# Performance work log

Measured on AMD Instinct MI355X. Metric: run time of the kernel, lower is better.

The kernel has to match this reference:

```python
import jax, jax.numpy as jnp
import numpy as np

def setup_inputs() -> dict:
    key = jax.random.key(0)
    k1, k2, k3, k4 = jax.random.split(key, 4)
    B, T, C, D = 4, 4096, 1024, 128
    x = jax.random.normal(k1, (B, T, C), dtype=jnp.float32)
    Wq = jax.random.normal(k2, (C, D), dtype=jnp.float32) * (C ** -0.5)
    Wk = jax.random.normal(k3, (C, D), dtype=jnp.float32) * (C ** -0.5)
    Wv = jax.random.normal(k4, (C, D), dtype=jnp.float32) * (C ** -0.5)
    return {"x": x, "Wq": Wq, "Wk": Wk, "Wv": Wv}

def reference(x, Wq, Wk, Wv):
    # x: [B,T,C]; Wq/Wk/Wv: [C,D] (nn.Linear bias=False => x @ W)
    B, T, C = x.shape
    q = jnp.einsum('btc,cd->btd', x, Wq)  # [B,T,D]
    k = jnp.einsum('btc,cd->btd', x, Wk)
    v = jnp.einsum('btc,cd->btd', x, Wv)
    dk = q.shape[-1]
    scale = dk ** -0.5
    w = jnp.einsum('btd,bsd->bts', q, k) * scale  # [B,T,T]
    causal = jnp.tril(jnp.ones((T, T), dtype=bool))
    w = jnp.where(causal, w, -jnp.inf)
    w = jax.nn.softmax(w, axis=-1)
    # dropout p=0.0 => identity
    attention = jnp.einsum('bts,bsd->btd', w, v)  # [B,T,D]
    return attention
```

## Files before the change

kernel.cpp:

```cpp
#include <hip/hip_runtime.h>
#include <stdint.h>

typedef __bf16 bf16_t;
typedef bf16_t bf16x8 __attribute__((ext_vector_type(8)));
typedef float f32x4 __attribute__((ext_vector_type(4)));
typedef unsigned short us8 __attribute__((ext_vector_type(8)));
typedef unsigned short us4 __attribute__((ext_vector_type(4)));

#define B_ 4
#define T_ 4096
#define C_ 1024
#define D_ 128

#define NCHUNK_PB 288
#define L2E 1.4426950408889634f

__device__ __forceinline__ uint16_t f2bf(float f) {
    union { float f; uint32_t u; } v; v.f = f;
    uint32_t u = v.u;
    uint32_t r = (u + 0x7fffu + ((u >> 16) & 1u)) >> 16;
    return (uint16_t)r;
}

__global__ __launch_bounds__(256) void prep_w(const float* __restrict__ Wq,
                                              const float* __restrict__ Wk,
                                              const float* __restrict__ Wv,
                                              uint16_t* __restrict__ WT) {
    int idx = blockIdx.x * 256 + threadIdx.x;
    if (idx >= 3 * D_ * C_) return;
    int w   = idx / (D_ * C_);
    int rem = idx - w * (D_ * C_);
    int n   = rem / C_;
    int k   = rem - n * C_;
    const float* W = (w == 0) ? Wq : (w == 1) ? Wk : Wv;
    WT[idx] = f2bf(W[(size_t)k * D_ + n]);
}

#define AST 40

__global__ __launch_bounds__(256) void qkv_gemm(const float* __restrict__ x,
                                                const uint16_t* __restrict__ WT,
                                                uint16_t* __restrict__ qb,
                                                uint16_t* __restrict__ kb,
                                                uint16_t* __restrict__ vT) {
    __shared__ __align__(16) uint16_t A_lds[32 * AST];
    __shared__ __align__(16) uint16_t W_lds[3][128 * AST];

    int tid  = threadIdx.x;
    int lane = tid & 63;
    int wave = tid >> 6;
    int quad = lane >> 4;
    int lx   = lane & 15;
    int wm   = wave >> 1, wn = wave & 1;
    int m0   = blockIdx.x * 32;

    f32x4 acc[3][4];
    for (int w = 0; w < 3; w++)
        for (int nf = 0; nf < 4; nf++)
            acc[w][nf] = (f32x4){0.f, 0.f, 0.f, 0.f};

    int arow = tid >> 3, acb = (tid & 7) * 4;

    for (int k0 = 0; k0 < C_; k0 += 32) {
        {
            float4 a = *(const float4*)(x + (size_t)(m0 + arow) * C_ + k0 + acb);
            us4 u;
            u[0] = f2bf(a.x); u[1] = f2bf(a.y); u[2] = f2bf(a.z); u[3] = f2bf(a.w);
            *(us4*)&A_lds[arow * AST + acb] = u;
        }
#pragma unroll
        for (int i = 0; i < 6; i++) {
            int f = i * 2048 + tid * 8;
            int w = f >> 12, n = (f >> 5) & 127, kk = f & 31;
            *(us8*)&W_lds[w][n * AST + kk] =
                *(const us8*)(WT + (size_t)w * (D_ * C_) + (size_t)n * C_ + k0 + kk);
        }
        __syncthreads();

        bf16x8 af = *(const bf16x8*)&A_lds[(wm * 16 + lx) * AST + quad * 8];
#pragma unroll
        for (int w = 0; w < 3; w++)
#pragma unroll
            for (int nf = 0; nf < 4; nf++) {
                bf16x8 bf = *(const bf16x8*)&W_lds[w][(wn * 64 + nf * 16 + lx) * AST + quad * 8];
                acc[w][nf] = __builtin_amdgcn_mfma_f32_16x16x32_bf16(af, bf, acc[w][nf], 0, 0, 0);
            }
        __syncthreads();
    }

    int mbase = m0 + wm * 16 + quad * 4;
#pragma unroll
    for (int nf = 0; nf < 4; nf++) {
        int n = wn * 64 + nf * 16 + lx;
#pragma unroll
        for (int r = 0; r < 4; r++)
            qb[(size_t)(mbase + r) * D_ + n] = f2bf(acc[0][nf][r]);
#pragma unroll
        for (int r = 0; r < 4; r++)
            kb[(size_t)(mbase + r) * D_ + n] = f2bf(acc[1][nf][r]);
        int batch = mbase >> 12;
        int t     = mbase & 4095;
        us4 pv;
        pv[0] = f2bf(acc[2][nf][0]);
        pv[1] = f2bf(acc[2][nf][1]);
        pv[2] = f2bf(acc[2][nf][2]);
        pv[3] = f2bf(acc[2][nf][3]);
        *(us4*)&vT[(size_t)batch * D_ * T_ + (size_t)n * T_ + t] = pv;
    }
}

#define KST 136
#define VST 72

__global__ __launch_bounds__(256) void attn(const uint16_t* __restrict__ qb,
                                            const uint16_t* __restrict__ kb,
                                            const uint16_t* __restrict__ vT,
                                            float* __restrict__ part,
                                            float* __restrict__ ml) {
    __shared__ __align__(16) uint16_t K_lds[64 * KST];
    __shared__ __align__(16) uint16_t V_lds[128 * VST];
    __shared__ __align__(16) uint16_t P_lds[4][16 * VST];

    int tid  = threadIdx.x;
    int lane = tid & 63;
    int wave = tid >> 6;
    int quad = lane >> 4;
    int lx   = lane & 15;

    int batch = blockIdx.x & 3;
    int L     = NCHUNK_PB - 1 - (blockIdx.x >> 2);
    int g = 0;
    while (g < 7 && 4 * (g + 1) * (g + 2) <= L) g++;
    int rem   = L - 4 * g * (g + 1);
    int jt    = 8 * g + rem / (g + 1);
    int chunk = rem - (rem / (g + 1)) * (g + 1);
    int lidx  = batch * NCHUNK_PB + L;

    int q0     = jt * 64;
    int st0    = chunk * 8;
    int ntiles = min(8, jt - st0 + 1);

    const float scale = 0.08838834764831845f;

    bf16x8 qf[4];
    {
        const uint16_t* qp = qb + (size_t)(batch * T_ + q0 + wave * 16 + lx) * D_ + quad * 8;
#pragma unroll
        for (int kc = 0; kc < 4; kc++) qf[kc] = *(const bf16x8*)(qp + kc * 32);
    }

    f32x4 o[8];
    for (int i = 0; i < 8; i++) o[i] = (f32x4){0.f, 0.f, 0.f, 0.f};
    float m_i[4], l_i[4];
    for (int r = 0; r < 4; r++) { m_i[r] = -INFINITY; l_i[r] = 0.f; }

    int krow = tid >> 2, kcb = (tid & 3) * 32;
    int vd   = tid >> 1, vsb = (tid & 1) * 32;

    for (int it = 0; it < ntiles; it++) {
        int s0 = (st0 + it) * 64;
        {
            const uint16_t* kp = kb + (size_t)(batch * T_ + s0 + krow) * D_ + kcb;
#pragma unroll
            for (int i = 0; i < 4; i++)
                *(us8*)&K_lds[krow * KST + kcb + i * 8] = *(const us8*)(kp + i * 8);
        }
        {
            const uint16_t* vp = vT + (size_t)batch * D_ * T_ + (size_t)vd * T_ + s0 + vsb;
#pragma unroll
            for (int i = 0; i < 4; i++)
                *(us8*)&V_lds[vd * VST + vsb + i * 8] = *(const us8*)(vp + i * 8);
        }
        __syncthreads();

        f32x4 s[4];
        for (int nf = 0; nf < 4; nf++) s[nf] = (f32x4){0.f, 0.f, 0.f, 0.f};
#pragma unroll
        for (int kc = 0; kc < 4; kc++)
#pragma unroll
            for (int nf = 0; nf < 4; nf++) {
                bf16x8 kf = *(const bf16x8*)&K_lds[(nf * 16 + lx) * KST + kc * 32 + quad * 8];
                s[nf] = __builtin_amdgcn_mfma_f32_16x16x32_bf16(qf[kc], kf, s[nf], 0, 0, 0);
            }

        int rowg = q0 + wave * 16 + quad * 4;
        float p[4][4];
        bool do_mask = (s0 + 63 > q0 + wave * 16);
#pragma unroll
        for (int nf = 0; nf < 4; nf++) {
            int colg = s0 + nf * 16 + lx;
#pragma unroll
            for (int r = 0; r < 4; r++) {
                float sv = s[nf][r] * scale;
                if (do_mask && (colg > rowg + r)) sv = -INFINITY;
                p[nf][r] = sv;
            }
        }

        float rm[4];
#pragma unroll
        for (int r = 0; r < 4; r++)
            rm[r] = fmaxf(fmaxf(p[0][r], p[1][r]), fmaxf(p[2][r], p[3][r]));
#pragma unroll
        for (int off = 1; off < 16; off <<= 1)
#pragma unroll
            for (int r = 0; r < 4; r++)
                rm[r] = fmaxf(rm[r], __shfl_xor(rm[r], off, 64));

        float alpha[4], rs[4];
#pragma unroll
        for (int r = 0; r < 4; r++) {
            float mn = fmaxf(m_i[r], rm[r]);
            alpha[r] = exp2f((m_i[r] - mn) * L2E);
            m_i[r]   = mn;
            float sum = 0.f;
#pragma unroll
            for (int nf = 0; nf < 4; nf++) {
                float e = exp2f((p[nf][r] - mn) * L2E);
                p[nf][r] = e;
                sum += e;
            }
            rs[r] = sum;
        }
#pragma unroll
        for (int off = 1; off < 16; off <<= 1)
#pragma unroll
            for (int r = 0; r < 4; r++)
                rs[r] += __shfl_xor(rs[r], off, 64);
#pragma unroll
        for (int r = 0; r < 4; r++) l_i[r] = l_i[r] * alpha[r] + rs[r];
#pragma unroll
        for (int i = 0; i < 8; i++)
#pragma unroll
            for (int r = 0; r < 4; r++) o[i][r] *= alpha[r];

#pragma unroll
        for (int nf = 0; nf < 4; nf++)
#pragma unroll
            for (int r = 0; r < 4; r++)
                P_lds[wave][(quad * 4 + r) * VST + nf * 16 + lx] = f2bf(p[nf][r]);

        bf16x8 pf[2];
        pf[0] = *(const bf16x8*)&P_lds[wave][lx * VST + quad * 8];
        pf[1] = *(const bf16x8*)&P_lds[wave][lx * VST + 32 + quad * 8];
#pragma unroll
        for (int nf = 0; nf < 8; nf++)
#pragma unroll
            for (int kc = 0; kc < 2; kc++) {
                bf16x8 vf = *(const bf16x8*)&V_lds[(nf * 16 + lx) * VST + kc * 32 + quad * 8];
                o[nf] = __builtin_amdgcn_mfma_f32_16x16x32_bf16(pf[kc], vf, o[nf], 0, 0, 0);
            }
        __syncthreads();
    }

    float* pp = part + (size_t)lidx * (64 * 128);
#pragma unroll
    for (int nf = 0; nf < 8; nf++)
#pragma unroll
        for (int r = 0; r < 4; r++) {
            int lrow = wave * 16 + quad * 4 + r;
            pp[lrow * 128 + nf * 16 + lx] = o[nf][r];
        }
    if (lx == 0) {
#pragma unroll
        for (int r = 0; r < 4; r++) {
            int lrow = wave * 16 + quad * 4 + r;
            ml[(size_t)lidx * 128 + lrow * 2]     = m_i[r];
            ml[(size_t)lidx * 128 + lrow * 2 + 1] = l_i[r];
        }
    }
}

__global__ __launch_bounds__(256) void combine(const float* __restrict__ part,
                                               const float* __restrict__ ml,
                                               float* __restrict__ out) {
    int bidx  = blockIdx.x;
    int batch = bidx >> 6;
    int jt    = bidx & 63;
    int g     = jt >> 3;
    int base  = batch * NCHUNK_PB + jt + g * (jt - 4 * g - 4);
    int nch   = g + 1;

    int tid  = threadIdx.x;
    int lrow = tid >> 2;
    int c0   = (tid & 3) * 32;

    float M = -INFINITY;
    for (int c = 0; c < nch; c++)
        M = fmaxf(M, ml[(size_t)(base + c) * 128 + lrow * 2]);

    float Lsum = 0.f;
    f32x4 acc[8];
#pragma unroll
    for (int i = 0; i < 8; i++) acc[i] = (f32x4){0.f, 0.f, 0.f, 0.f};

    for (int c = 0; c < nch; c++) {
        float m = ml[(size_t)(base + c) * 128 + lrow * 2];
        float l = ml[(size_t)(base + c) * 128 + lrow * 2 + 1];
        float w = exp2f((m - M) * L2E);
        Lsum += l * w;
        const float* p = part + (size_t)(base + c) * (64 * 128) + lrow * 128 + c0;
#pragma unroll
        for (int i = 0; i < 8; i++) {
            f32x4 v = *(const f32x4*)(p + i * 4);
            acc[i] += v * w;
        }
    }
    float inv = 1.f / Lsum;
    size_t row = (size_t)(batch * T_ + jt * 64 + lrow);
#pragma unroll
    for (int i = 0; i < 8; i++)
        *(f32x4*)(out + row * 128 + c0 + i * 4) = acc[i] * inv;
}

extern "C" void kernel_launch(void* const* d_in, const int* in_sizes, int n_in,
                              void* d_out, int out_size, void* d_ws, size_t ws_size,
                              hipStream_t stream) {
    const float* x  = (const float*)d_in[0];
    const float* Wq = (const float*)d_in[1];
    const float* Wk = (const float*)d_in[2];
    const float* Wv = (const float*)d_in[3];
    float* out = (float*)d_out;

    uint16_t* ws = (uint16_t*)d_ws;
    uint16_t* qb = ws;
    uint16_t* kb = qb + (size_t)16384 * 128;
    uint16_t* vT = kb + (size_t)16384 * 128;
    uint16_t* WT = vT + (size_t)16384 * 128;
    float* part = (float*)(WT + (size_t)3 * D_ * C_);
    float* ml   = part + (size_t)4 * NCHUNK_PB * 64 * 128;

    prep_w<<<dim3((3 * D_ * C_ + 255) / 256), dim3(256), 0, stream>>>(Wq, Wk, Wv, WT);
    qkv_gemm<<<dim3(16384 / 32), dim3(256), 0, stream>>>(x, WT, qb, kb, vT);
    attn<<<dim3(B_ * NCHUNK_PB), dim3(256), 0, stream>>>(qb, kb, vT, part, ml);
    combine<<<dim3(B_ * (T_ / 64)), dim3(256), 0, stream>>>(part, ml, out);
}
```

Before: 219.5 us.

## Retile QKV GEMM per weight, fold scale into Q, compute row sums via MFMA

The QKV projection now gives each block a 64-row tile and a single weight matrix, with K steps of 64. x is converted to bf16 using byte perms with round-half-up. The softmax scale and log2(e) are folded into Q at projection time, so the attention loop uses exp2 directly and only applies the causal mask on the diagonal tile. The per-row exp sums are no longer done with a shuffle reduction but by an extra MFMA column against a ones row appended to V in LDS. P is packed two bf16 per 32-bit LDS store. The trade-offs are that x is now read three times across blocks, an extra MFMA tile runs per step, and the rounding mode changes slightly.

```diff
diff --git a/kernel.cpp b/kernel.cpp
--- a/kernel.cpp
+++ b/kernel.cpp
@@ -6,6 +6,7 @@
 typedef float f32x4 __attribute__((ext_vector_type(4)));
 typedef unsigned short us8 __attribute__((ext_vector_type(8)));
 typedef unsigned short us4 __attribute__((ext_vector_type(4)));
+typedef unsigned int u32x4 __attribute__((ext_vector_type(4)));
 
 #define B_ 4
 #define T_ 4096
@@ -13,13 +14,17 @@
 #define D_ 128
 
 #define NCHUNK_PB 288
-#define L2E 1.4426950408889634f
+#define QSCALE 0.12751744f
 
 __device__ __forceinline__ uint16_t f2bf(float f) {
     union { float f; uint32_t u; } v; v.f = f;
     uint32_t u = v.u;
     uint32_t r = (u + 0x7fffu + ((u >> 16) & 1u)) >> 16;
     return (uint16_t)r;
+}
+
+__device__ __forceinline__ uint16_t bfru(float f) {
+    return (uint16_t)((__float_as_uint(f) + 0x8000u) >> 16);
 }
 
 __global__ __launch_bounds__(256) void prep_w(const float* __restrict__ Wq,
@@ -36,15 +41,15 @@
     WT[idx] = f2bf(W[(size_t)k * D_ + n]);
 }
 
-#define AST 40
+#define GST 72
 
 __global__ __launch_bounds__(256) void qkv_gemm(const float* __restrict__ x,
                                                 const uint16_t* __restrict__ WT,
                                                 uint16_t* __restrict__ qb,
                                                 uint16_t* __restrict__ kb,
                                                 uint16_t* __restrict__ vT) {
-    __shared__ __align__(16) uint16_t A_lds[32 * AST];
-    __shared__ __align__(16) uint16_t W_lds[3][128 * AST];
+    __shared__ __align__(16) uint16_t A_lds[64 * GST];
+    __shared__ __align__(16) uint16_t W_lds[128 * GST];
 
     int tid  = threadIdx.x;
     int lane = tid & 63;
@@ -52,60 +57,89 @@
     int quad = lane >> 4;
     int lx   = lane & 15;
     int wm   = wave >> 1, wn = wave & 1;
-    int m0   = blockIdx.x * 32;
-
-    f32x4 acc[3][4];
-    for (int w = 0; w < 3; w++)
+
+    int bx   = blockIdx.x;
+    int wsel = bx % 3;
+    int m0   = (bx / 3) * 64;
+    const uint16_t* Wp = WT + (size_t)wsel * (D_ * C_);
+
+    f32x4 acc[2][4];
+    for (int mf = 0; mf < 2; mf++)
         for (int nf = 0; nf < 4; nf++)
-            acc[w][nf] = (f32x4){0.f, 0.f, 0.f, 0.f};
-
-    int arow = tid >> 3, acb = (tid & 7) * 4;
-
-    for (int k0 = 0; k0 < C_; k0 += 32) {
+            acc[mf][nf] = (f32x4){0.f, 0.f, 0.f, 0.f};
+
+    int arow = tid >> 2, acb = (tid & 3) * 16;
+    int wrow = tid >> 1, wcb = (tid & 1) * 32;
+
+    for (int k0 = 0; k0 < C_; k0 += 64) {
         {
-            float4 a = *(const float4*)(x + (size_t)(m0 + arow) * C_ + k0 + acb);
-            us4 u;
-            u[0] = f2bf(a.x); u[1] = f2bf(a.y); u[2] = f2bf(a.z); u[3] = f2bf(a.w);
-            *(us4*)&A_lds[arow * AST + acb] = u;
-        }
-#pragma unroll
-        for (int i = 0; i < 6; i++) {
-            int f = i * 2048 + tid * 8;
-            int w = f >> 12, n = (f >> 5) & 127, kk = f & 31;
-            *(us8*)&W_lds[w][n * AST + kk] =
-                *(const us8*)(WT + (size_t)w * (D_ * C_) + (size_t)n * C_ + k0 + kk);
+            const float* xp = x + (size_t)(m0 + arow) * C_ + k0 + acb;
+            uint32_t d[8];
+#pragma unroll
+            for (int j = 0; j < 4; j++) {
+                float4 f = *(const float4*)(xp + j * 4);
+                uint32_t u0 = __float_as_uint(f.x) + 0x8000u;
+                uint32_t u1 = __float_as_uint(f.y) + 0x8000u;
+                uint32_t u2 = __float_as_uint(f.z) + 0x8000u;
+                uint32_t u3 = __float_as_uint(f.w) + 0x8000u;
+                d[2 * j]     = __builtin_amdgcn_perm(u1, u0, 0x07060302);
+                d[2 * j + 1] = __builtin_amdgcn_perm(u3, u2, 0x07060302);
+            }
+            *(u32x4*)&A_lds[arow * GST + acb]     = (u32x4){d[0], d[1], d[2], d[3]};
+            *(u32x4*)&A_lds[arow * GST + acb + 8] = (u32x4){d[4], d[5], d[6], d[7]};
+        }
+        {
+            const uint16_t* wp = Wp + (size_t)wrow * C_ + k0 + wcb;
+#pragma unroll
+            for (int i = 0; i < 4; i++)
+                *(us8*)&W_lds[wrow * GST + wcb + i * 8] = *(const us8*)(wp + i * 8);
         }
         __syncthreads();
 
-        bf16x8 af = *(const bf16x8*)&A_lds[(wm * 16 + lx) * AST + quad * 8];
-#pragma unroll
-        for (int w = 0; w < 3; w++)
-#pragma unroll
-            for (int nf = 0; nf < 4; nf++) {
-                bf16x8 bf = *(const bf16x8*)&W_lds[w][(wn * 64 + nf * 16 + lx) * AST + quad * 8];
-                acc[w][nf] = __builtin_amdgcn_mfma_f32_16x16x32_bf16(af, bf, acc[w][nf], 0, 0, 0);
-            }
+#pragma unroll
+        for (int kc = 0; kc < 2; kc++) {
+            bf16x8 af[2];
+#pragma unroll
+            for (int mf = 0; mf < 2; mf++)
+                af[mf] = *(const bf16x8*)&A_lds[(wm * 32 + mf * 16 + lx) * GST + kc * 32 + quad * 8];
+#pragma unroll
+            for (int nf = 0; nf < 4; nf++) {
+                bf16x8 bf = *(const bf16x8*)&W_lds[(wn * 64 + nf * 16 + lx) * GST + kc * 32 + quad * 8];
+                acc[0][nf] = __builtin_amdgcn_mfma_f32_16x16x32_bf16(af[0], bf, acc[0][nf], 0, 0, 0);
+                acc[1][nf] = __builtin_amdgcn_mfma_f32_16x16x32_bf16(af[1], bf, acc[1][nf], 0, 0, 0);
+            }
+        }
         __syncthreads();
     }
 
-    int mbase = m0 + wm * 16 + quad * 4;
-#pragma unroll
-    for (int nf = 0; nf < 4; nf++) {
-        int n = wn * 64 + nf * 16 + lx;
-#pragma unroll
-        for (int r = 0; r < 4; r++)
-            qb[(size_t)(mbase + r) * D_ + n] = f2bf(acc[0][nf][r]);
-#pragma unroll
-        for (int r = 0; r < 4; r++)
-            kb[(size_t)(mbase + r) * D_ + n] = f2bf(acc[1][nf][r]);
-        int batch = mbase >> 12;
-        int t     = mbase & 4095;
-        us4 pv;
-        pv[0] = f2bf(acc[2][nf][0]);
-        pv[1] = f2bf(acc[2][nf][1]);
-        pv[2] = f2bf(acc[2][nf][2]);
-        pv[3] = f2bf(acc[2][nf][3]);
-        *(us4*)&vT[(size_t)batch * D_ * T_ + (size_t)n * T_ + t] = pv;
+    int mrow0 = m0 + wm * 32 + quad * 4;
+    if (wsel == 2) {
+#pragma unroll
+        for (int mf = 0; mf < 2; mf++) {
+            int mbase = mrow0 + mf * 16;
+            int batch = mbase >> 12;
+            int t     = mbase & 4095;
+#pragma unroll
+            for (int nf = 0; nf < 4; nf++) {
+                int n = wn * 64 + nf * 16 + lx;
+                us4 pv;
+#pragma unroll
+                for (int r = 0; r < 4; r++) pv[r] = bfru(acc[mf][nf][r]);
+                *(us4*)&vT[(size_t)batch * D_ * T_ + (size_t)n * T_ + t] = pv;
+            }
+        }
+    } else {
+        uint16_t* dst = (wsel == 0) ? qb : kb;
+        float sc = (wsel == 0) ? QSCALE : 1.0f;
+#pragma unroll
+        for (int mf = 0; mf < 2; mf++)
+#pragma unroll
+            for (int nf = 0; nf < 4; nf++) {
+                int n = wn * 64 + nf * 16 + lx;
+#pragma unroll
+                for (int r = 0; r < 4; r++)
+                    dst[(size_t)(mrow0 + mf * 16 + r) * D_ + n] = bfru(acc[mf][nf][r] * sc);
+            }
     }
 }
 
@@ -118,7 +152,7 @@
                                             float* __restrict__ part,
                                             float* __restrict__ ml) {
     __shared__ __align__(16) uint16_t K_lds[64 * KST];
-    __shared__ __align__(16) uint16_t V_lds[128 * VST];
+    __shared__ __align__(16) uint16_t V_lds[144 * VST];
     __shared__ __align__(16) uint16_t P_lds[4][16 * VST];
 
     int tid  = threadIdx.x;
@@ -140,7 +174,10 @@
     int st0    = chunk * 8;
     int ntiles = min(8, jt - st0 + 1);
 
-    const float scale = 0.08838834764831845f;
+    for (int i = tid; i < 16 * VST; i += 256) {
+        int r = i / VST;
+        V_lds[(128 + r) * VST + (i - r * VST)] = (r == 0) ? 0x3F80 : 0;
+    }
 
     bf16x8 qf[4];
     {
@@ -149,10 +186,10 @@
         for (int kc = 0; kc < 4; kc++) qf[kc] = *(const bf16x8*)(qp + kc * 32);
     }
 
-    f32x4 o[8];
-    for (int i = 0; i < 8; i++) o[i] = (f32x4){0.f, 0.f, 0.f, 0.f};
-    float m_i[4], l_i[4];
-    for (int r = 0; r < 4; r++) { m_i[r] = -INFINITY; l_i[r] = 0.f; }
+    f32x4 o[9];
+    for (int i = 0; i < 9; i++) o[i] = (f32x4){0.f, 0.f, 0.f, 0.f};
+    float m_i[4];
+    for (int r = 0; r < 4; r++) m_i[r] = -INFINITY;
 
     int krow = tid >> 2, kcb = (tid & 3) * 32;
     int vd   = tid >> 1, vsb = (tid & 1) * 32;
@@ -183,17 +220,20 @@
                 s[nf] = __builtin_amdgcn_mfma_f32_16x16x32_bf16(qf[kc], kf, s[nf], 0, 0, 0);
             }
 
-        int rowg = q0 + wave * 16 + quad * 4;
         float p[4][4];
-        bool do_mask = (s0 + 63 > q0 + wave * 16);
-#pragma unroll
-        for (int nf = 0; nf < 4; nf++) {
-            int colg = s0 + nf * 16 + lx;
-#pragma unroll
-            for (int r = 0; r < 4; r++) {
-                float sv = s[nf][r] * scale;
-                if (do_mask && (colg > rowg + r)) sv = -INFINITY;
-                p[nf][r] = sv;
+#pragma unroll
+        for (int nf = 0; nf < 4; nf++)
+#pragma unroll
+            for (int r = 0; r < 4; r++) p[nf][r] = s[nf][r];
+
+        if (st0 + it == jt) {
+            int rowg = q0 + wave * 16 + quad * 4;
+#pragma unroll
+            for (int nf = 0; nf < 4; nf++) {
+                int colg = s0 + nf * 16 + lx;
+#pragma unroll
+                for (int r = 0; r < 4; r++)
+                    if (colg > rowg + r) p[nf][r] = -INFINITY;
             }
         }
 
@@ -207,44 +247,37 @@
             for (int r = 0; r < 4; r++)
                 rm[r] = fmaxf(rm[r], __shfl_xor(rm[r], off, 64));
 
-        float alpha[4], rs[4];
+        float alpha[4];
 #pragma unroll
         for (int r = 0; r < 4; r++) {
             float mn = fmaxf(m_i[r], rm[r]);
-            alpha[r] = exp2f((m_i[r] - mn) * L2E);
+            alpha[r] = exp2f(m_i[r] - mn);
             m_i[r]   = mn;
-            float sum = 0.f;
-#pragma unroll
-            for (int nf = 0; nf < 4; nf++) {
-                float e = exp2f((p[nf][r] - mn) * L2E);
-                p[nf][r] = e;
-                sum += e;
-            }
-            rs[r] = sum;
-        }
-#pragma unroll
-        for (int off = 1; off < 16; off <<= 1)
-#pragma unroll
-            for (int r = 0; r < 4; r++)
-                rs[r] += __shfl_xor(rs[r], off, 64);
-#pragma unroll
-        for (int r = 0; r < 4; r++) l_i[r] = l_i[r] * alpha[r] + rs[r];
-#pragma unroll
-        for (int i = 0; i < 8; i++)
+#pragma unroll
+            for (int nf = 0; nf < 4; nf++)
+                p[nf][r] = exp2f(p[nf][r] - mn);
+        }
+#pragma unroll
+        for (int i = 0; i < 9; i++)
 #pragma unroll
             for (int r = 0; r < 4; r++) o[i][r] *= alpha[r];
 
 #pragma unroll
         for (int nf = 0; nf < 4; nf++)
 #pragma unroll
-            for (int r = 0; r < 4; r++)
-                P_lds[wave][(quad * 4 + r) * VST + nf * 16 + lx] = f2bf(p[nf][r]);
+            for (int r = 0; r < 4; r++) {
+                uint32_t u  = __float_as_uint(p[nf][r]) + 0x8000u;
+                uint32_t pu = (uint32_t)__shfl_xor((int)u, 1, 64);
+                uint32_t pk = __builtin_amdgcn_perm(pu, u, 0x07060302);
+                if ((lane & 1) == 0)
+                    *(uint32_t*)&P_lds[wave][(quad * 4 + r) * VST + nf * 16 + lx] = pk;
+            }
 
         bf16x8 pf[2];
         pf[0] = *(const bf16x8*)&P_lds[wave][lx * VST + quad * 8];
         pf[1] = *(const bf16x8*)&P_lds[wave][lx * VST + 32 + quad * 8];
 #pragma unroll
-        for (int nf = 0; nf < 8; nf++)
+        for (int nf = 0; nf < 9; nf++)
 #pragma unroll
             for (int kc = 0; kc < 2; kc++) {
                 bf16x8 vf = *(const bf16x8*)&V_lds[(nf * 16 + lx) * VST + kc * 32 + quad * 8];
@@ -266,7 +299,7 @@
         for (int r = 0; r < 4; r++) {
             int lrow = wave * 16 + quad * 4 + r;
             ml[(size_t)lidx * 128 + lrow * 2]     = m_i[r];
-            ml[(size_t)lidx * 128 + lrow * 2 + 1] = l_i[r];
+            ml[(size_t)lidx * 128 + lrow * 2 + 1] = o[8][r];
         }
     }
 }
@@ -297,7 +330,7 @@
     for (int c = 0; c < nch; c++) {
         float m = ml[(size_t)(base + c) * 128 + lrow * 2];
         float l = ml[(size_t)(base + c) * 128 + lrow * 2 + 1];
-        float w = exp2f((m - M) * L2E);
+        float w = exp2f(m - M);
         Lsum += l * w;
         const float* p = part + (size_t)(base + c) * (64 * 128) + lrow * 128 + c0;
 #pragma unroll
@@ -331,7 +364,7 @@
     float* ml   = part + (size_t)4 * NCHUNK_PB * 64 * 128;
 
     prep_w<<<dim3((3 * D_ * C_ + 255) / 256), dim3(256), 0, stream>>>(Wq, Wk, Wv, WT);
-    qkv_gemm<<<dim3(16384 / 32), dim3(256), 0, stream>>>(x, WT, qb, kb, vT);
+    qkv_gemm<<<dim3(3 * (16384 / 64)), dim3(256), 0, stream>>>(x, WT, qb, kb, vT);
     attn<<<dim3(B_ * NCHUNK_PB), dim3(256), 0, stream>>>(qb, kb, vT, part, ml);
     combine<<<dim3(B_ * (T_ / 64)), dim3(256), 0, stream>>>(part, ml, out);
 }
```

Measured after the change: 210.8 us. 4.0% less time.
